# Performance work log

Hardware: AMD Instinct MI355X
Metric: run time of the kernel (lower is better)

## Reference

```python
import jax, jax.numpy as jnp
import numpy as np
from jax import lax

LOOKBACK = 336
N_FEATURES = 164
HORIZON = 96
D_MODEL = 64
D_STATE = 16
D_CONV = 4
EXPAND = 2
D_INNER = EXPAND * D_MODEL  # 128
DT_RANK = (D_MODEL + 15) // 16  # 4
MLP_HIDDEN = 64
BATCH = 512


def setup_inputs() -> dict:
    key = jax.random.key(0)
    ks = jax.random.split(key, 20)
    f32 = jnp.float32
    inp = {}
    inp["x_raw"] = jax.random.normal(ks[0], (BATCH, LOOKBACK), f32)
    inp["x_features"] = jax.random.normal(ks[1], (BATCH, N_FEATURES), f32)
    # embed Linear(1, d_model)
    inp["embed_W"] = jax.random.normal(ks[2], (1, D_MODEL), f32) * 0.5
    inp["embed_b"] = jnp.zeros((D_MODEL,), f32)
    # Mamba params (mamba-ssm layout, stored as [in, out] for matmul)
    inp["in_W"] = jax.random.normal(ks[3], (D_MODEL, 2 * D_INNER), f32) * (1.0 / np.sqrt(D_MODEL))
    inp["conv_W"] = jax.random.normal(ks[4], (D_INNER, D_CONV), f32) * 0.3
    inp["conv_b"] = jnp.zeros((D_INNER,), f32)
    inp["xproj_W"] = jax.random.normal(ks[5], (D_INNER, DT_RANK + 2 * D_STATE), f32) * (1.0 / np.sqrt(D_INNER))
    inp["dt_W"] = jax.random.normal(ks[6], (DT_RANK, D_INNER), f32) * (1.0 / np.sqrt(DT_RANK))
    inp["dt_b"] = jax.random.uniform(ks[7], (D_INNER,), f32, -4.0, -2.0)  # softplus -> small dt
    # A_log init = log(arange(1..d_state)) broadcast over d_inner, as in mamba-ssm
    inp["A_log"] = jnp.log(jnp.broadcast_to(jnp.arange(1, D_STATE + 1, dtype=f32), (D_INNER, D_STATE)))
    inp["D"] = jnp.ones((D_INNER,), f32)
    inp["out_W"] = jax.random.normal(ks[8], (D_INNER, D_MODEL), f32) * (1.0 / np.sqrt(D_INNER))
    # MLP stream
    inp["mlp_W1"] = jax.random.normal(ks[9], (N_FEATURES, MLP_HIDDEN), f32) * (1.0 / np.sqrt(N_FEATURES))
    inp["mlp_b1"] = jnp.zeros((MLP_HIDDEN,), f32)
    inp["mlp_W2"] = jax.random.normal(ks[10], (MLP_HIDDEN, MLP_HIDDEN // 2), f32) * (1.0 / np.sqrt(MLP_HIDDEN))
    inp["mlp_b2"] = jnp.zeros((MLP_HIDDEN // 2,), f32)
    # prediction head
    fin = D_MODEL + MLP_HIDDEN // 2
    inp["head_W"] = jax.random.normal(ks[11], (fin, HORIZON), f32) * (1.0 / np.sqrt(fin))
    inp["head_b"] = jnp.zeros((HORIZON,), f32)
    return inp


def silu(x):
    return x * jax.nn.sigmoid(x)


def mamba_block(u, in_W, conv_W, conv_b, xproj_W, dt_W, dt_b, A_log, D, out_W):
    # u: [B, L, d_model]
    B_, L, _ = u.shape
    xz = u @ in_W                      # [B, L, 2*D_INNER]
    x, z = jnp.split(xz, 2, axis=-1)   # each [B, L, D_INNER]
    # causal depthwise conv1d (pad left d_conv-1), then SiLU
    xc = x.transpose(0, 2, 1)          # [B, D_INNER, L]
    kern = conv_W[:, None, :]          # [D_INNER, 1, K] (OIH)
    xc = lax.conv_general_dilated(xc, kern, window_strides=(1,),
                                  padding=[(D_CONV - 1, 0)],
                                  dimension_numbers=("NCH", "OIH", "NCH"),
                                  feature_group_count=D_INNER)
    xc = silu(xc + conv_b[None, :, None])
    x = xc.transpose(0, 2, 1)          # [B, L, D_INNER]
    # input-dependent SSM params
    x_dbl = x @ xproj_W                # [B, L, DT_RANK + 2*D_STATE]
    dt = x_dbl[..., :DT_RANK]
    Bm = x_dbl[..., DT_RANK:DT_RANK + D_STATE]          # [B, L, N]
    Cm = x_dbl[..., DT_RANK + D_STATE:]                 # [B, L, N]
    delta = jax.nn.softplus(dt @ dt_W + dt_b)           # [B, L, D_INNER]
    A = -jnp.exp(A_log)                                 # [D_INNER, N]

    # selective scan over time
    def step(h, inps):
        d_t, B_t, C_t, x_t = inps  # [B,Di], [B,N], [B,N], [B,Di]
        dA = jnp.exp(d_t[:, :, None] * A[None])              # [B, Di, N]
        dBx = (d_t * x_t)[:, :, None] * B_t[:, None, :]      # [B, Di, N]
        h = dA * h + dBx
        y_t = jnp.einsum("bdn,bn->bd", h, C_t)
        return h, y_t

    h0 = jnp.zeros((B_, D_INNER, D_STATE), u.dtype)
    seq = (delta.transpose(1, 0, 2), Bm.transpose(1, 0, 2),
           Cm.transpose(1, 0, 2), x.transpose(1, 0, 2))
    _, ys = lax.scan(step, h0, seq)        # ys: [L, B, D_INNER]
    y = ys.transpose(1, 0, 2) + x * D[None, None, :]
    y = y * silu(z)
    return y @ out_W                        # [B, L, d_model]


def reference(x_raw, x_features, embed_W, embed_b, in_W, conv_W, conv_b,
              xproj_W, dt_W, dt_b, A_log, D, out_W,
              mlp_W1, mlp_b1, mlp_W2, mlp_b2, head_W, head_b):
    # embed raw series: [B, L] -> [B, L, 1] -> [B, L, d_model]
    h = x_raw[..., None] @ embed_W + embed_b
    h = mamba_block(h, in_W, conv_W, conv_b, xproj_W, dt_W, dt_b, A_log, D, out_W)
    h_mamba_out = h[:, -1, :]                       # [B, d_model]
    h_mlp = jax.nn.relu(x_features @ mlp_W1 + mlp_b1) @ mlp_W2 + mlp_b2
    h_final = jnp.concatenate([h_mamba_out, h_mlp], axis=1)
    return h_final @ head_W + head_b                # [B, horizon]
```

## Files before the change

### kernel.cpp

```cpp
#include <hip/hip_runtime.h>
#include <math.h>

#define LOOKBACK 336
#define NFEAT    164
#define HORIZON  96
#define DMODEL   64
#define DSTATE   16
#define DINNER   128
#define MLPH     64
#define BATCH    512
#define XCP      132
#define NG       4
#define GSEG     84
#define CHK      12
#define NCH      7

typedef float v2f __attribute__((ext_vector_type(2)));

__device__ __forceinline__ float fast_rcp(float x) { return __builtin_amdgcn_rcpf(x); }
__device__ __forceinline__ float silu_f(float x) {
    return x * fast_rcp(1.f + __expf(-x));
}

__global__ __launch_bounds__(512, 2) void mamba_one(
    const float* __restrict__ x_raw,   const float* __restrict__ x_features,
    const float* __restrict__ embed_W, const float* __restrict__ embed_b,
    const float* __restrict__ in_W,
    const float* __restrict__ conv_W,  const float* __restrict__ conv_b,
    const float* __restrict__ xproj_W, const float* __restrict__ dt_W,
    const float* __restrict__ dt_b,    const float* __restrict__ A_log,
    const float* __restrict__ Dvec,    const float* __restrict__ out_W,
    const float* __restrict__ mlp_W1,  const float* __restrict__ mlp_b1,
    const float* __restrict__ mlp_W2,  const float* __restrict__ mlp_b2,
    const float* __restrict__ head_W,  const float* __restrict__ head_b,
    float* __restrict__ out)
{
    __shared__ __align__(16) float xrl[344];
    __shared__ __align__(16) float xprojT[20*XCP];
    __shared__ __align__(16) float xcbuf[2][NG][CHK*XCP];
    __shared__ __align__(16) float Bsh[NG][CHK][DSTATE];
    __shared__ __align__(16) float dtraw[NG][CHK][4];
    __shared__ float xcl[DINNER], zsil[DINNER], Cl[DSTATE], yv[DINNER];
    __shared__ float hfin[96], mlph[MLPH];

    const int tid = threadIdx.x;
    const int b   = blockIdx.x;
    const int g   = tid >> 7;
    const int ch  = tid & 127;

    for (int i = tid; i < 339; i += 512)
        xrl[i] = (i >= 3) ? x_raw[b*LOOKBACK + i - 3] : 0.f;
    for (int idx = tid; idx < 20*DINNER; idx += 512) {
        int jj = idx >> 7, d = idx & 127;
        xprojT[jj*XCP + d] = xproj_W[d*36 + jj];
    }

    float w1 = 0.f, w0 = 0.f;
    for (int dm = 0; dm < DMODEL; ++dm) {
        float w = in_W[dm*(2*DINNER) + ch];
        w1 = fmaf(embed_W[dm], w, w1);
        w0 = fmaf(embed_b[dm], w, w0);
    }
    const float4 cw = *(const float4*)&conv_W[ch*4];
    const float  cb = conv_b[ch];
    const float dtw0 = dt_W[ch],       dtw1 = dt_W[128 + ch],
                dtw2 = dt_W[256 + ch], dtw3 = dt_W[384 + ch];
    const float dtb_r = dt_b[ch];
    bool structured = true;
    #pragma unroll
    for (int i = 0; i < 16; ++i) {
        float a = __expf(A_log[ch*DSTATE + i]);
        float ex = (float)(i + 1);
        structured = structured && (fabsf(a - ex) < 1e-3f * ex);
    }
    const bool sfast = __all(structured);
    __syncthreads();

    {
        float* xw = &xcbuf[0][g][0];
        const float* xr = &xrl[g*GSEG];
        if (g == 0) {
            for (int tt = 0; tt < CHK; ++tt) {
                float acc = cb;
                if (tt >= 3) acc = fmaf(fmaf(xr[tt],   w1, w0), cw.x, acc);
                if (tt >= 2) acc = fmaf(fmaf(xr[tt+1], w1, w0), cw.y, acc);
                if (tt >= 1) acc = fmaf(fmaf(xr[tt+2], w1, w0), cw.z, acc);
                acc = fmaf(fmaf(xr[tt+3], w1, w0), cw.w, acc);
                xw[tt*XCP + ch] = silu_f(acc);
            }
        } else {
            float e0 = fmaf(xr[0], w1, w0);
            float e1 = fmaf(xr[1], w1, w0);
            float e2 = fmaf(xr[2], w1, w0);
            #pragma unroll
            for (int tt = 0; tt < CHK; ++tt) {
                float e3 = fmaf(xr[tt+3], w1, w0);
                float acc = cb + e0*cw.x + e1*cw.y + e2*cw.z + e3*cw.w;
                xw[tt*XCP + ch] = silu_f(acc);
                e0 = e1; e1 = e2; e2 = e3;
            }
        }
    }
    __syncthreads();

    v2f h01={0,0},h23={0,0},h45={0,0},h67={0,0},
        h89={0,0},hAB={0,0},hCD={0,0},hEF={0,0};
    float dacc = 0.f;

    for (int c = 0; c < NCH; ++c) {
        const int buf = c & 1;

        if (ch < 60) {
            const int tg = ch / 10;
            const int j0 = (ch - tg*10) * 2;
            const int t0 = tg*2;
            const float* p0 = &xprojT[j0*XCP];
            const float* p1 = &xprojT[(j0+1)*XCP];
            const float* x0 = &xcbuf[buf][g][t0*XCP];
            const float* x1 = &xcbuf[buf][g][(t0+1)*XCP];
            v2f a00 = {0,0}, a01 = {0,0}, a10 = {0,0}, a11 = {0,0};
            #pragma unroll 8
            for (int d = 0; d < DINNER; d += 4) {
                float4 xv0 = *(const float4*)(x0 + d);
                float4 xv1 = *(const float4*)(x1 + d);
                float4 q0  = *(const float4*)(p0 + d);
                float4 q1  = *(const float4*)(p1 + d);
                v2f x0l = {xv0.x, xv0.y}, x0h = {xv0.z, xv0.w};
                v2f x1l = {xv1.x, xv1.y}, x1h = {xv1.z, xv1.w};
                v2f q0l = {q0.x, q0.y},   q0h = {q0.z, q0.w};
                v2f q1l = {q1.x, q1.y},   q1h = {q1.z, q1.w};
                a00 = __builtin_elementwise_fma(x0l, q0l, a00);
                a00 = __builtin_elementwise_fma(x0h, q0h, a00);
                a01 = __builtin_elementwise_fma(x0l, q1l, a01);
                a01 = __builtin_elementwise_fma(x0h, q1h, a01);
                a10 = __builtin_elementwise_fma(x1l, q0l, a10);
                a10 = __builtin_elementwise_fma(x1h, q0h, a10);
                a11 = __builtin_elementwise_fma(x1l, q1l, a11);
                a11 = __builtin_elementwise_fma(x1h, q1h, a11);
            }
            float r00 = a00.x + a00.y, r01 = a01.x + a01.y;
            float r10 = a10.x + a10.y, r11 = a11.x + a11.y;
            if (j0 < 4) {
                *(float2*)&dtraw[g][t0][j0]   = make_float2(r00, r01);
                *(float2*)&dtraw[g][t0+1][j0] = make_float2(r10, r11);
            } else {
                *(float2*)&Bsh[g][t0][j0-4]   = make_float2(r00, r01);
                *(float2*)&Bsh[g][t0+1][j0-4] = make_float2(r10, r11);
            }
        }
        __syncthreads();

        const float* xs = &xcbuf[buf][g][0];
        if (__builtin_expect(sfast, 1)) {
            #pragma unroll
            for (int tt = 0; tt < CHK; ++tt) {
                float4 dr = *(const float4*)&dtraw[g][tt][0];
                float dv = fmaf(dr.x, dtw0, fmaf(dr.y, dtw1,
                           fmaf(dr.z, dtw2, fmaf(dr.w, dtw3, dtb_r))));
                float e  = __expf(dv);
                float p  = 1.f + e;
                float r  = fast_rcp(p);
                float dl = (dv > 80.f) ? dv : __logf(p);
                dacc += dl;
                float ux = dl * xs[tt*XCP + ch];
                float4 B0 = *(const float4*)&Bsh[g][tt][0];
                float4 B1 = *(const float4*)&Bsh[g][tt][4];
                float4 B2 = *(const float4*)&Bsh[g][tt][8];
                float4 B3 = *(const float4*)&Bsh[g][tt][12];
                float r2 = r*r;
                v2f r2v = {r2, r2};
                v2f p01 = {r, r2};
                v2f p23 = p01*r2v, p45 = p23*r2v, p67 = p45*r2v, p89 = p67*r2v,
                    pAB = p89*r2v, pCD = pAB*r2v, pEF = pCD*r2v;
                v2f uxv = {ux, ux};
                h01 = __builtin_elementwise_fma(p01, h01, uxv*(v2f){B0.x,B0.y});
                h23 = __builtin_elementwise_fma(p23, h23, uxv*(v2f){B0.z,B0.w});
                h45 = __builtin_elementwise_fma(p45, h45, uxv*(v2f){B1.x,B1.y});
                h67 = __builtin_elementwise_fma(p67, h67, uxv*(v2f){B1.z,B1.w});
                h89 = __builtin_elementwise_fma(p89, h89, uxv*(v2f){B2.x,B2.y});
                hAB = __builtin_elementwise_fma(pAB, hAB, uxv*(v2f){B2.z,B2.w});
                hCD = __builtin_elementwise_fma(pCD, hCD, uxv*(v2f){B3.x,B3.y});
                hEF = __builtin_elementwise_fma(pEF, hEF, uxv*(v2f){B3.z,B3.w});
            }
        } else {
            const float* Arow = A_log + ch*DSTATE;
            for (int tt = 0; tt < CHK; ++tt) {
                float4 dr = *(const float4*)&dtraw[g][tt][0];
                float dv = fmaf(dr.x, dtw0, fmaf(dr.y, dtw1,
                           fmaf(dr.z, dtw2, fmaf(dr.w, dtw3, dtb_r))));
                float e  = __expf(dv);
                float dl = (dv > 15.f) ? dv : __logf(1.f + e);
                dacc += dl;
                float ux = dl * xs[tt*XCP + ch];
                const float* Br = &Bsh[g][tt][0];
                float hv[16] = {h01.x,h01.y,h23.x,h23.y,h45.x,h45.y,h67.x,h67.y,
                                h89.x,h89.y,hAB.x,hAB.y,hCD.x,hCD.y,hEF.x,hEF.y};
                for (int i = 0; i < 16; ++i)
                    hv[i] = fmaf(__expf(-__expf(Arow[i])*dl), hv[i], ux*Br[i]);
                h01=(v2f){hv[0],hv[1]};   h23=(v2f){hv[2],hv[3]};
                h45=(v2f){hv[4],hv[5]};   h67=(v2f){hv[6],hv[7]};
                h89=(v2f){hv[8],hv[9]};   hAB=(v2f){hv[10],hv[11]};
                hCD=(v2f){hv[12],hv[13]}; hEF=(v2f){hv[14],hv[15]};
            }
        }

        if (c + 1 < NCH) {
            float* xw = &xcbuf[buf^1][g][0];
            const float* xr = &xrl[g*GSEG + (c+1)*CHK];
            float e0 = fmaf(xr[0], w1, w0);
            float e1 = fmaf(xr[1], w1, w0);
            float e2 = fmaf(xr[2], w1, w0);
            float v = 0.f;
            #pragma unroll
            for (int tt = 0; tt < CHK; ++tt) {
                float e3 = fmaf(xr[tt+3], w1, w0);
                float acc = cb + e0*cw.x + e1*cw.y + e2*cw.z + e3*cw.w;
                v = silu_f(acc);
                xw[tt*XCP + ch] = v;
                e0 = e1; e1 = e2; e2 = e3;
            }
            if (g == NG-1 && c + 1 == NCH-1) xcl[ch] = v;
        }
        __syncthreads();
    }

    float* hpart = &xcbuf[0][0][0];
    float* dsum  = hpart + 16*512;
    {
        const int gid = g*128 + ch;
        float hv[16] = {h01.x,h01.y,h23.x,h23.y,h45.x,h45.y,h67.x,h67.y,
                        h89.x,h89.y,hAB.x,hAB.y,hCD.x,hCD.y,hEF.x,hEF.y};
        #pragma unroll
        for (int i = 0; i < 16; ++i) hpart[i*512 + gid] = hv[i];
        dsum[gid] = dacc;
    }
    __syncthreads();

    float H[16];
    if (tid < 128) {
        #pragma unroll
        for (int i = 0; i < 16; ++i) H[i] = hpart[i*512 + tid];
        for (int gg = 1; gg < NG; ++gg) {
            float D = dsum[gg*128 + tid];
            if (structured) {
                float r = __expf(-D);
                float pw = 1.f;
                #pragma unroll
                for (int i = 0; i < 16; ++i) {
                    pw *= r;
                    H[i] = fmaf(pw, H[i], hpart[i*512 + gg*128 + tid]);
                }
            } else {
                #pragma unroll
                for (int i = 0; i < 16; ++i)
                    H[i] = fmaf(__expf(-__expf(A_log[tid*DSTATE+i])*D),
                                H[i], hpart[i*512 + gg*128 + tid]);
            }
        }
    } else if (tid < 256) {
        const int c2 = tid - 128;
        float a1 = 0.f, a0 = 0.f;
        for (int dm = 0; dm < DMODEL; ++dm) {
            float w = in_W[dm*(2*DINNER) + DINNER + c2];
            a1 = fmaf(embed_W[dm], w, a1);
            a0 = fmaf(embed_b[dm], w, a0);
        }
        float zv = fmaf(xrl[338], a1, a0);
        zsil[c2] = silu_f(zv);
    } else if (tid < 320) {
        const int lane = tid - 256;
        const int n = lane & 15, q = lane >> 4;
        float acc = 0.f;
        for (int d = q*32; d < q*32 + 32; ++d)
            acc = fmaf(xcl[d], xproj_W[d*36 + 20 + n], acc);
        acc += __shfl_xor(acc, 16);
        acc += __shfl_xor(acc, 32);
        if (lane < 16) Cl[n] = acc;
    } else if (tid >= 384) {
        const int lane = tid - 384;
        const int j = lane >> 1, k = lane & 1;
        const float* xf = x_features + b*NFEAT;
        float acc = 0.f;
        const int f0 = k*82, f1 = (k ? NFEAT : 82);
        for (int f = f0; f < f1; ++f)
            acc = fmaf(xf[f], mlp_W1[f*MLPH + j], acc);
        acc += __shfl_xor(acc, 1);
        if (k == 0) mlph[j] = fmaxf(acc + mlp_b1[j], 0.f);
    }
    __syncthreads();

    if (tid < 128) {
        float acc = 0.f;
        #pragma unroll
        for (int i = 0; i < 16; ++i) acc = fmaf(H[i], Cl[i], acc);
        float y = acc + xcl[tid]*Dvec[tid];
        yv[tid] = y * zsil[tid];
    } else if (tid < 192) {
        const int lane = tid - 128;
        const int j = lane >> 1, k = lane & 1;
        float acc = 0.f;
        for (int kk = k*32; kk < k*32 + 32; ++kk)
            acc = fmaf(mlph[kk], mlp_W2[kk*32 + j], acc);
        acc += __shfl_xor(acc, 1);
        if (k == 0) hfin[64 + j] = acc + mlp_b2[j];
    }
    __syncthreads();

    if (tid < 256) {
        const int o = tid >> 2, k = tid & 3;
        float acc = 0.f;
        for (int d = k*32; d < k*32 + 32; ++d)
            acc = fmaf(yv[d], out_W[d*DMODEL + o], acc);
        acc += __shfl_xor(acc, 1);
        acc += __shfl_xor(acc, 2);
        if (k == 0) hfin[o] = acc;
    }
    __syncthreads();

    if (tid < 192) {
        const int o = tid >> 1, k = tid & 1;
        float acc = 0.f;
        for (int i = k*48; i < k*48 + 48; ++i)
            acc = fmaf(hfin[i], head_W[i*HORIZON + o], acc);
        acc += __shfl_xor(acc, 1);
        if (k == 0) out[b*HORIZON + o] = acc + head_b[o];
    }
}

extern "C" void kernel_launch(void* const* d_in, const int* in_sizes, int n_in,
                              void* d_out, int out_size, void* d_ws, size_t ws_size,
                              hipStream_t stream) {
    (void)in_sizes; (void)n_in; (void)out_size; (void)d_ws; (void)ws_size;
    mamba_one<<<BATCH, 512, 0, stream>>>(
        (const float*)d_in[0],  (const float*)d_in[1],  (const float*)d_in[2],
        (const float*)d_in[3],  (const float*)d_in[4],  (const float*)d_in[5],
        (const float*)d_in[6],  (const float*)d_in[7],  (const float*)d_in[8],
        (const float*)d_in[9],  (const float*)d_in[10], (const float*)d_in[11],
        (const float*)d_in[12], (const float*)d_in[13], (const float*)d_in[14],
        (const float*)d_in[15], (const float*)d_in[16], (const float*)d_in[17],
        (const float*)d_in[18], (float*)d_out);
}
```

Before: 173.9 us.

## Software-pipeline x_proj with scan using triple-buffered conv and double-buffered B/dt

Reorganizes the per-chunk loop into a three-stage pipeline. The conv for chunk c+2 and the x_proj for chunk c+1 are computed in the same phase as the scan of chunk c. This removes one __syncthreads per chunk. Chunk size drops from 12 to 7 (now 12 chunks), and x_proj work alternates between half-warps so its cost is spread out. The trade-off is more shared memory (triple-buffered xc, double-buffered Bsh and dtraw), more chunk iterations, and a partially idle x_proj pair mapping for the odd chunk length.

```diff
diff --git a/kernel.cpp b/kernel.cpp
--- a/kernel.cpp
+++ b/kernel.cpp
@@ -12,8 +12,8 @@
 #define XCP      132
 #define NG       4
 #define GSEG     84
-#define CHK      12
-#define NCH      7
+#define CHK      7
+#define NCH      12
 
 typedef float v2f __attribute__((ext_vector_type(2)));
 
@@ -37,9 +37,9 @@
 {
     __shared__ __align__(16) float xrl[344];
     __shared__ __align__(16) float xprojT[20*XCP];
-    __shared__ __align__(16) float xcbuf[2][NG][CHK*XCP];
-    __shared__ __align__(16) float Bsh[NG][CHK][DSTATE];
-    __shared__ __align__(16) float dtraw[NG][CHK][4];
+    __shared__ __align__(16) float xc3[3][NG][CHK*XCP];
+    __shared__ __align__(16) float Bsh2[2][NG][CHK][DSTATE];
+    __shared__ __align__(16) float dtraw2[2][NG][CHK][4];
     __shared__ float xcl[DINNER], zsil[DINNER], Cl[DSTATE], yv[DINNER];
     __shared__ float hfin[96], mlph[MLPH];
 
@@ -76,10 +76,11 @@
     const bool sfast = __all(structured);
     __syncthreads();
 
-    {
-        float* xw = &xcbuf[0][g][0];
-        const float* xr = &xrl[g*GSEG];
-        if (g == 0) {
+    auto conv_chunk = [&](int k) {
+        float* xw = &xc3[k % 3][g][0];
+        const float* xr = &xrl[g*GSEG + k*CHK];
+        if (g == 0 && k == 0) {
+            #pragma unroll
             for (int tt = 0; tt < CHK; ++tt) {
                 float acc = cb;
                 if (tt >= 3) acc = fmaf(fmaf(xr[tt],   w1, w0), cw.x, acc);
@@ -92,15 +93,71 @@
             float e0 = fmaf(xr[0], w1, w0);
             float e1 = fmaf(xr[1], w1, w0);
             float e2 = fmaf(xr[2], w1, w0);
+            float v = 0.f;
             #pragma unroll
             for (int tt = 0; tt < CHK; ++tt) {
                 float e3 = fmaf(xr[tt+3], w1, w0);
                 float acc = cb + e0*cw.x + e1*cw.y + e2*cw.z + e3*cw.w;
-                xw[tt*XCP + ch] = silu_f(acc);
+                v = silu_f(acc);
+                xw[tt*XCP + ch] = v;
                 e0 = e1; e1 = e2; e2 = e3;
             }
-        }
-    }
+            if (g == NG-1 && k == NCH-1) xcl[ch] = v;
+        }
+    };
+
+    auto a2_chunk = [&](int k) {
+        if ((ch >> 6) == (k & 1)) {
+            const int lane = ch & 63;
+            if (lane < 40) {
+                const int tg = lane / 10;
+                const int j0 = (lane - tg*10) * 2;
+                const int t0 = tg*2;
+                const int t1 = (t0+1 < CHK) ? t0+1 : t0;
+                const int p  = k & 1;
+                const float* p0 = &xprojT[j0*XCP];
+                const float* p1 = &xprojT[(j0+1)*XCP];
+                const float* x0 = &xc3[k % 3][g][t0*XCP];
+                const float* x1 = &xc3[k % 3][g][t1*XCP];
+                v2f a00 = {0,0}, a01 = {0,0}, a10 = {0,0}, a11 = {0,0};
+                #pragma unroll 8
+                for (int d = 0; d < DINNER; d += 4) {
+                    float4 xv0 = *(const float4*)(x0 + d);
+                    float4 xv1 = *(const float4*)(x1 + d);
+                    float4 q0  = *(const float4*)(p0 + d);
+                    float4 q1  = *(const float4*)(p1 + d);
+                    v2f x0l = {xv0.x, xv0.y}, x0h = {xv0.z, xv0.w};
+                    v2f x1l = {xv1.x, xv1.y}, x1h = {xv1.z, xv1.w};
+                    v2f q0l = {q0.x, q0.y},   q0h = {q0.z, q0.w};
+                    v2f q1l = {q1.x, q1.y},   q1h = {q1.z, q1.w};
+                    a00 = __builtin_elementwise_fma(x0l, q0l, a00);
+                    a00 = __builtin_elementwise_fma(x0h, q0h, a00);
+                    a01 = __builtin_elementwise_fma(x0l, q1l, a01);
+                    a01 = __builtin_elementwise_fma(x0h, q1h, a01);
+                    a10 = __builtin_elementwise_fma(x1l, q0l, a10);
+                    a10 = __builtin_elementwise_fma(x1h, q0h, a10);
+                    a11 = __builtin_elementwise_fma(x1l, q1l, a11);
+                    a11 = __builtin_elementwise_fma(x1h, q1h, a11);
+                }
+                float r00 = a00.x + a00.y, r01 = a01.x + a01.y;
+                float r10 = a10.x + a10.y, r11 = a11.x + a11.y;
+                if (j0 < 4) {
+                    *(float2*)&dtraw2[p][g][t0][j0] = make_float2(r00, r01);
+                    if (t1 != t0)
+                        *(float2*)&dtraw2[p][g][t1][j0] = make_float2(r10, r11);
+                } else {
+                    *(float2*)&Bsh2[p][g][t0][j0-4] = make_float2(r00, r01);
+                    if (t1 != t0)
+                        *(float2*)&Bsh2[p][g][t1][j0-4] = make_float2(r10, r11);
+                }
+            }
+        }
+    };
+
+    conv_chunk(0);
+    __syncthreads();
+    a2_chunk(0);
+    conv_chunk(1);
     __syncthreads();
 
     v2f h01={0,0},h23={0,0},h45={0,0},h67={0,0},
@@ -108,65 +165,25 @@
     float dacc = 0.f;
 
     for (int c = 0; c < NCH; ++c) {
-        const int buf = c & 1;
-
-        if (ch < 60) {
-            const int tg = ch / 10;
-            const int j0 = (ch - tg*10) * 2;
-            const int t0 = tg*2;
-            const float* p0 = &xprojT[j0*XCP];
-            const float* p1 = &xprojT[(j0+1)*XCP];
-            const float* x0 = &xcbuf[buf][g][t0*XCP];
-            const float* x1 = &xcbuf[buf][g][(t0+1)*XCP];
-            v2f a00 = {0,0}, a01 = {0,0}, a10 = {0,0}, a11 = {0,0};
-            #pragma unroll 8
-            for (int d = 0; d < DINNER; d += 4) {
-                float4 xv0 = *(const float4*)(x0 + d);
-                float4 xv1 = *(const float4*)(x1 + d);
-                float4 q0  = *(const float4*)(p0 + d);
-                float4 q1  = *(const float4*)(p1 + d);
-                v2f x0l = {xv0.x, xv0.y}, x0h = {xv0.z, xv0.w};
-                v2f x1l = {xv1.x, xv1.y}, x1h = {xv1.z, xv1.w};
-                v2f q0l = {q0.x, q0.y},   q0h = {q0.z, q0.w};
-                v2f q1l = {q1.x, q1.y},   q1h = {q1.z, q1.w};
-                a00 = __builtin_elementwise_fma(x0l, q0l, a00);
-                a00 = __builtin_elementwise_fma(x0h, q0h, a00);
-                a01 = __builtin_elementwise_fma(x0l, q1l, a01);
-                a01 = __builtin_elementwise_fma(x0h, q1h, a01);
-                a10 = __builtin_elementwise_fma(x1l, q0l, a10);
-                a10 = __builtin_elementwise_fma(x1h, q0h, a10);
-                a11 = __builtin_elementwise_fma(x1l, q1l, a11);
-                a11 = __builtin_elementwise_fma(x1h, q1h, a11);
-            }
-            float r00 = a00.x + a00.y, r01 = a01.x + a01.y;
-            float r10 = a10.x + a10.y, r11 = a11.x + a11.y;
-            if (j0 < 4) {
-                *(float2*)&dtraw[g][t0][j0]   = make_float2(r00, r01);
-                *(float2*)&dtraw[g][t0+1][j0] = make_float2(r10, r11);
-            } else {
-                *(float2*)&Bsh[g][t0][j0-4]   = make_float2(r00, r01);
-                *(float2*)&Bsh[g][t0+1][j0-4] = make_float2(r10, r11);
-            }
-        }
-        __syncthreads();
-
-        const float* xs = &xcbuf[buf][g][0];
+        const int p  = c & 1;
+        const float* xs = &xc3[c % 3][g][0];
+
         if (__builtin_expect(sfast, 1)) {
             #pragma unroll
             for (int tt = 0; tt < CHK; ++tt) {
-                float4 dr = *(const float4*)&dtraw[g][tt][0];
+                float4 dr = *(const float4*)&dtraw2[p][g][tt][0];
                 float dv = fmaf(dr.x, dtw0, fmaf(dr.y, dtw1,
                            fmaf(dr.z, dtw2, fmaf(dr.w, dtw3, dtb_r))));
                 float e  = __expf(dv);
-                float p  = 1.f + e;
-                float r  = fast_rcp(p);
-                float dl = (dv > 80.f) ? dv : __logf(p);
+                float pp = 1.f + e;
+                float r  = fast_rcp(pp);
+                float dl = (dv > 80.f) ? dv : __logf(pp);
                 dacc += dl;
                 float ux = dl * xs[tt*XCP + ch];
-                float4 B0 = *(const float4*)&Bsh[g][tt][0];
-                float4 B1 = *(const float4*)&Bsh[g][tt][4];
-                float4 B2 = *(const float4*)&Bsh[g][tt][8];
-                float4 B3 = *(const float4*)&Bsh[g][tt][12];
+                float4 B0 = *(const float4*)&Bsh2[p][g][tt][0];
+                float4 B1 = *(const float4*)&Bsh2[p][g][tt][4];
+                float4 B2 = *(const float4*)&Bsh2[p][g][tt][8];
+                float4 B3 = *(const float4*)&Bsh2[p][g][tt][12];
                 float r2 = r*r;
                 v2f r2v = {r2, r2};
                 v2f p01 = {r, r2};
@@ -185,14 +202,14 @@
         } else {
             const float* Arow = A_log + ch*DSTATE;
             for (int tt = 0; tt < CHK; ++tt) {
-                float4 dr = *(const float4*)&dtraw[g][tt][0];
+                float4 dr = *(const float4*)&dtraw2[p][g][tt][0];
                 float dv = fmaf(dr.x, dtw0, fmaf(dr.y, dtw1,
                            fmaf(dr.z, dtw2, fmaf(dr.w, dtw3, dtb_r))));
                 float e  = __expf(dv);
                 float dl = (dv > 15.f) ? dv : __logf(1.f + e);
                 dacc += dl;
                 float ux = dl * xs[tt*XCP + ch];
-                const float* Br = &Bsh[g][tt][0];
+                const float* Br = &Bsh2[p][g][tt][0];
                 float hv[16] = {h01.x,h01.y,h23.x,h23.y,h45.x,h45.y,h67.x,h67.y,
                                 h89.x,h89.y,hAB.x,hAB.y,hCD.x,hCD.y,hEF.x,hEF.y};
                 for (int i = 0; i < 16; ++i)
@@ -204,27 +221,12 @@
             }
         }
 
-        if (c + 1 < NCH) {
-            float* xw = &xcbuf[buf^1][g][0];
-            const float* xr = &xrl[g*GSEG + (c+1)*CHK];
-            float e0 = fmaf(xr[0], w1, w0);
-            float e1 = fmaf(xr[1], w1, w0);
-            float e2 = fmaf(xr[2], w1, w0);
-            float v = 0.f;
-            #pragma unroll
-            for (int tt = 0; tt < CHK; ++tt) {
-                float e3 = fmaf(xr[tt+3], w1, w0);
-                float acc = cb + e0*cw.x + e1*cw.y + e2*cw.z + e3*cw.w;
-                v = silu_f(acc);
-                xw[tt*XCP + ch] = v;
-                e0 = e1; e1 = e2; e2 = e3;
-            }
-            if (g == NG-1 && c + 1 == NCH-1) xcl[ch] = v;
-        }
+        if (c + 1 < NCH) a2_chunk(c + 1);
+        if (c + 2 < NCH) conv_chunk(c + 2);
         __syncthreads();
     }
 
-    float* hpart = &xcbuf[0][0][0];
+    float* hpart = &xc3[0][0][0];
     float* dsum  = hpart + 16*512;
     {
         const int gid = g*128 + ch;
```

Measured after the change: 240.1 us. +38.0%, slower.
